# Performance work log

Hardware: AMD Instinct MI355X
Metric: run time of the kernel (lower is better)

Reference implementation:

```python
import math
import jax, jax.numpy as jnp
import numpy as np
from jax import lax

N, L = 256, 4096
DIM_LINEAR, DIM_CONV, KERNEL, STRIDE = 64, 128, 15, 1


def setup_inputs() -> dict:
    key = jax.random.key(0)
    ks = jax.random.split(key, 10)
    tokens = jax.random.randint(ks[0], (N, L), 0, 4, dtype=jnp.int32)
    emb = jax.random.normal(ks[1], (4, DIM_LINEAR), dtype=jnp.float32)
    conv_w = jax.random.normal(ks[2], (DIM_CONV, DIM_LINEAR, KERNEL), dtype=jnp.float32) * (1.0 / math.sqrt(DIM_LINEAR * KERNEL))
    conv_b = jax.random.normal(ks[3], (DIM_CONV,), dtype=jnp.float32) * 0.01
    s = 1.0 / math.sqrt(DIM_CONV)
    Wq = jax.random.normal(ks[4], (DIM_CONV, DIM_CONV), dtype=jnp.float32) * s
    bq = jax.random.normal(ks[5], (DIM_CONV,), dtype=jnp.float32) * 0.01
    Wk = jax.random.normal(ks[6], (DIM_CONV, DIM_CONV), dtype=jnp.float32) * s
    bk = jax.random.normal(ks[7], (DIM_CONV,), dtype=jnp.float32) * 0.01
    Wv = jax.random.normal(ks[8], (DIM_CONV, DIM_CONV), dtype=jnp.float32) * s
    bv = jax.random.normal(ks[9], (DIM_CONV,), dtype=jnp.float32) * 0.01
    return {"tokens": tokens, "emb": emb, "conv_w": conv_w, "conv_b": conv_b,
            "Wq": Wq, "bq": bq, "Wk": Wk, "bk": bk, "Wv": Wv, "bv": bv}


def reference(tokens, emb, conv_w, conv_b, Wq, bq, Wk, bk, Wv, bv):
    # embedding: [N, L, dl] -> channels-first [N, dl, L]
    x = emb[tokens].transpose(0, 2, 1)
    # conv1d, valid padding: [N, dc, Lout]
    y = lax.conv_general_dilated(x, conv_w, window_strides=(STRIDE,),
                                 padding='VALID',
                                 dimension_numbers=('NCH', 'OIH', 'NCH'))
    y = y + conv_b[None, :, None]
    read = y.transpose(0, 2, 1)                      # [N, Lout, dc]
    read_mean = read.mean(axis=1)                    # [N, dc]
    q = read_mean @ Wq.T + bq                        # [N, dc]
    k = read @ Wk.T + bk                             # [N, Lout, dc]
    v = read @ Wv.T + bv                             # [N, Lout, dc]
    scores = jnp.einsum('nd,nld->nl', q, k) / math.sqrt(DIM_CONV)
    attn = jax.nn.softmax(scores, axis=1)            # [N, Lout]
    out = jnp.einsum('nl,nld->nd', attn, v)          # [N, dc]
    return out
```

## Files before the change

### kernel.cpp

```cpp
#include <hip/hip_runtime.h>
#include <math.h>

#define NN 256
#define LL 4096
#define DL 64
#define DC 128
#define KS 15
#define LOUT (LL - KS + 1)
#define CST 133
#define RSQRT_DC 0.08838834764831843f

__global__ __launch_bounds__(128) void contrib_kernel(const float* __restrict__ emb,
                                                      const float* __restrict__ conv_w,
                                                      float* __restrict__ ctb) {
    const int c = blockIdx.x;
    const int tid = threadIdx.x;
    __shared__ float ws[DL][16];
    __shared__ float es[4][DL];
    const float* wsrc = conv_w + (size_t)c * (DL * KS);
    for (int idx = tid; idx < DL * KS; idx += 128) ws[idx / KS][idx % KS] = wsrc[idx];
    for (int idx = tid; idx < 4 * DL; idx += 128) es[idx >> 6][idx & 63] = emb[idx];
    __syncthreads();
    if (tid < 60) {
        const int v = tid / KS, k = tid % KS;
        float s = 0.f;
#pragma unroll
        for (int i = 0; i < DL; ++i) s += es[v][i] * ws[i][k];
        ctb[tid * DC + c] = s;
    }
}

__device__ __forceinline__ float block_sum(float v, float* red8, int tid) {
#pragma unroll
    for (int off = 32; off > 0; off >>= 1) v += __shfl_down(v, off, 64);
    if ((tid & 63) == 0) red8[tid >> 6] = v;
    __syncthreads();
    float r = ((red8[0] + red8[1]) + (red8[2] + red8[3])) +
              ((red8[4] + red8[5]) + (red8[6] + red8[7]));
    __syncthreads();
    return r;
}

__device__ __forceinline__ float block_max(float v, float* red8, int tid) {
#pragma unroll
    for (int off = 32; off > 0; off >>= 1) v = fmaxf(v, __shfl_down(v, off, 64));
    if ((tid & 63) == 0) red8[tid >> 6] = v;
    __syncthreads();
    float r = fmaxf(fmaxf(fmaxf(red8[0], red8[1]), fmaxf(red8[2], red8[3])),
                    fmaxf(fmaxf(red8[4], red8[5]), fmaxf(red8[6], red8[7])));
    __syncthreads();
    return r;
}

__global__ __launch_bounds__(512) void encoder_kernel(
    const int* __restrict__ tokens, const float* __restrict__ ctb_g,
    const float* __restrict__ conv_b,
    const float* __restrict__ Wq, const float* __restrict__ bq,
    const float* __restrict__ Wk, const float* __restrict__ bk,
    const float* __restrict__ Wv, const float* __restrict__ bv,
    float* __restrict__ out) {
    const int n = blockIdx.x;
    const int tid = threadIdx.x;

    __shared__ __align__(16) float esc[16 + LL];
    __shared__ unsigned tok2[258];
    __shared__ float ctb[60 * CST];
    __shared__ float Tt[4 * 256];
    __shared__ float rm[DC], qv[DC], qk[DC], zv[DC];
    __shared__ float stab[60], cf[60], Acc[60];
    __shared__ float red8[8];
    __shared__ int totw[4][4];
    __shared__ int cnt[KS][4];

#define TOK2(p) ((tok2[(p) >> 4] >> (2 * ((p) & 15))) & 3u)

    for (int i = tid; i < 16 + LL; i += 512) esc[i] = 0.f;
    if (tid < 60) Acc[tid] = 0.f;
    if (tid < 2) tok2[256 + tid] = 0u;
    for (int idx = tid; idx < 60 * DC; idx += 512)
        ctb[(idx >> 7) * CST + (idx & 127)] = ctb_g[idx];

    if (tid < 256) {
        const int4* tv = (const int4*)(tokens + (size_t)n * LL) + tid * 4;
        unsigned w = 0;
#pragma unroll
        for (int m = 0; m < 4; ++m) {
            int4 t4 = tv[m];
            w |= ((unsigned)t4.x | ((unsigned)t4.y << 2) |
                  ((unsigned)t4.z << 4) | ((unsigned)t4.w << 6)) << (8 * m);
        }
        tok2[tid] = w;
        int c0, c1, c2, c3;
        {
            unsigned y, z;
            y = w;                      z = (y | (y >> 1)) & 0x55555555u; c0 = 16 - __popc(z);
            y = w ^ 0x55555555u;        z = (y | (y >> 1)) & 0x55555555u; c1 = 16 - __popc(z);
            y = w ^ 0xAAAAAAAAu;        z = (y | (y >> 1)) & 0x55555555u; c2 = 16 - __popc(z);
            y = w ^ 0xFFFFFFFFu;        z = (y | (y >> 1)) & 0x55555555u; c3 = 16 - __popc(z);
        }
#pragma unroll
        for (int off = 32; off > 0; off >>= 1) {
            c0 += __shfl_down(c0, off, 64); c1 += __shfl_down(c1, off, 64);
            c2 += __shfl_down(c2, off, 64); c3 += __shfl_down(c3, off, 64);
        }
        if ((tid & 63) == 0) {
            const int wv = tid >> 6;
            totw[wv][0] = c0; totw[wv][1] = c1; totw[wv][2] = c2; totw[wv][3] = c3;
        }
    }
    __syncthreads();

    if (tid < KS) {
        const int k = tid;
        int h0 = 0, h1 = 0, h2 = 0, h3 = 0;
        for (int p = 0; p < k; ++p) {
            int v = (int)TOK2(p);
            h0 += (v == 0); h1 += (v == 1); h2 += (v == 2); h3 += (v == 3);
        }
        for (int p = k + LOUT; p < LL; ++p) {
            int v = (int)TOK2(p);
            h0 += (v == 0); h1 += (v == 1); h2 += (v == 2); h3 += (v == 3);
        }
        cnt[k][0] = (totw[0][0] + totw[1][0] + totw[2][0] + totw[3][0]) - h0;
        cnt[k][1] = (totw[0][1] + totw[1][1] + totw[2][1] + totw[3][1]) - h1;
        cnt[k][2] = (totw[0][2] + totw[1][2] + totw[2][2] + totw[3][2]) - h2;
        cnt[k][3] = (totw[0][3] + totw[1][3] + totw[2][3] + totw[3][3]) - h3;
    }
    __syncthreads();
    if (tid < 60) cf[tid] = (float)cnt[tid % KS][tid / KS];
    __syncthreads();

    if (tid < DC) {
        float s = 0.f;
#pragma unroll
        for (int j = 0; j < 60; ++j) s += cf[j] * ctb[j * CST + tid];
        rm[tid] = conv_b[tid] + s * (1.0f / (float)LOUT);
    }
    __syncthreads();

    if (tid < DC) {
        const float4* wr = (const float4*)(Wq + (size_t)tid * DC);
        const float4* r4 = (const float4*)rm;
        float s = 0.f;
#pragma unroll
        for (int j = 0; j < DC / 4; ++j) {
            float4 w = wr[j], r = r4[j];
            s += w.x * r.x + w.y * r.y + w.z * r.z + w.w * r.w;
        }
        qv[tid] = s + bq[tid];
    }
    __syncthreads();

    if (tid < DC) {
        float s = 0.f;
        for (int c = 0; c < DC; ++c) s += qv[c] * Wk[(size_t)c * DC + tid];
        qk[tid] = s;
    }
    __syncthreads();

    if (tid < 60) {
        float s = 0.f;
#pragma unroll
        for (int c = 0; c < DC; ++c) s += ctb[tid * CST + c] * qk[c];
        stab[tid] = s * RSQRT_DC;
    }
    float term = 0.f;
    if (tid < DC) term = conv_b[tid] * qk[tid] + qv[tid] * bk[tid];
    const float base = block_sum(term, red8, tid) * RSQRT_DC;

    for (int e = tid; e < 1024; e += 512) {
        const int j = e >> 8, b = e & 255;
        float s = stab[(b & 3) * KS + 4 * j] +
                  stab[((b >> 2) & 3) * KS + 4 * j + 1] +
                  stab[((b >> 4) & 3) * KS + 4 * j + 2];
        if (j < 3) s += stab[((b >> 6) & 3) * KS + 4 * j + 3];
        Tt[e] = s;
    }
    __syncthreads();

    const unsigned d0 = tok2[tid >> 1];
    const unsigned d1 = tok2[(tid >> 1) + 1];
    const unsigned long long W = (unsigned long long)d0 | ((unsigned long long)d1 << 32);
    const int sbase = (tid & 1) << 4;
    const int t0 = tid * 8;
    float lmax = -3.4e38f;
    {
        float sreg[8];
#pragma unroll
        for (int p = 0; p < 8; ++p) {
            const unsigned w = (unsigned)(W >> (sbase + 2 * p));
            sreg[p] = base + Tt[w & 255] + Tt[256 + ((w >> 8) & 255)] +
                      Tt[512 + ((w >> 16) & 255)] + Tt[768 + ((w >> 24) & 63)];
        }
#pragma unroll
        for (int p = 0; p < 8; ++p) {
            if (t0 + p < LOUT) { esc[16 + t0 + p] = sreg[p]; lmax = fmaxf(lmax, sreg[p]); }
        }
    }
    const float m = block_max(lmax, red8, tid);

    float lsum = 0.f;
    for (int t = tid; t < LOUT; t += 512) {
        float e = __expf(esc[16 + t] - m);
        esc[16 + t] = e;
        lsum += e;
    }
    const float S = block_sum(lsum, red8, tid);
    const float invS = 1.0f / S;

    {
        float ew[24];
        const float4* ep = (const float4*)(esc + t0);
#pragma unroll
        for (int i = 0; i < 6; ++i) {
            float4 f = ep[i];
            ew[4 * i] = f.x; ew[4 * i + 1] = f.y; ew[4 * i + 2] = f.z; ew[4 * i + 3] = f.w;
        }
        float a1[KS], a2[KS], a3[KS];
#pragma unroll
        for (int k = 0; k < KS; ++k) { a1[k] = 0.f; a2[k] = 0.f; a3[k] = 0.f; }
#pragma unroll
        for (int p = 0; p < 8; ++p) {
            const int v = (int)((W >> (sbase + 2 * p)) & 3ull);
            const float m1 = (v == 1) ? 1.f : 0.f;
            const float m2 = (v == 2) ? 1.f : 0.f;
            const float m3 = (v == 3) ? 1.f : 0.f;
#pragma unroll
            for (int k = 0; k < KS; ++k) {
                const float e = ew[16 + p - k];
                a1[k] += m1 * e; a2[k] += m2 * e; a3[k] += m3 * e;
            }
        }
        const int lane = tid & 63;
#pragma unroll
        for (int k = 0; k < KS; ++k) {
            float v1 = a1[k], v2 = a2[k], v3 = a3[k];
#pragma unroll
            for (int off = 32; off > 0; off >>= 1) {
                v1 += __shfl_down(v1, off, 64);
                v2 += __shfl_down(v2, off, 64);
                v3 += __shfl_down(v3, off, 64);
            }
            if (lane == 0) {
                atomicAdd(&Acc[KS + k], v1);
                atomicAdd(&Acc[2 * KS + k], v2);
                atomicAdd(&Acc[3 * KS + k], v3);
            }
        }
    }
    __syncthreads();
    if (tid < KS) Acc[tid] = S - Acc[KS + tid] - Acc[2 * KS + tid] - Acc[3 * KS + tid];
    __syncthreads();

    if (tid < DC) {
        float s = 0.f;
#pragma unroll
        for (int j = 0; j < 60; ++j) s += Acc[j] * ctb[j * CST + tid];
        zv[tid] = conv_b[tid] + s * invS;
    }
    __syncthreads();

    if (tid < DC) {
        const float4* wr = (const float4*)(Wv + (size_t)tid * DC);
        const float4* z4 = (const float4*)zv;
        float s = 0.f;
#pragma unroll
        for (int j = 0; j < DC / 4; ++j) {
            float4 w = wr[j], z = z4[j];
            s += w.x * z.x + w.y * z.y + w.z * z.z + w.w * z.w;
        }
        out[(size_t)n * DC + tid] = s + bv[tid];
    }
#undef TOK2
}

extern "C" void kernel_launch(void* const* d_in, const int* in_sizes, int n_in,
                              void* d_out, int out_size, void* d_ws, size_t ws_size,
                              hipStream_t stream) {
    const int*   tokens = (const int*)d_in[0];
    const float* emb    = (const float*)d_in[1];
    const float* conv_w = (const float*)d_in[2];
    const float* conv_b = (const float*)d_in[3];
    const float* Wq     = (const float*)d_in[4];
    const float* bq     = (const float*)d_in[5];
    const float* Wk     = (const float*)d_in[6];
    const float* bk     = (const float*)d_in[7];
    const float* Wv     = (const float*)d_in[8];
    const float* bv     = (const float*)d_in[9];
    float* out = (float*)d_out;
    float* ctb = (float*)d_ws;

    contrib_kernel<<<DC, 128, 0, stream>>>(emb, conv_w, ctb);
    encoder_kernel<<<NN, 512, 0, stream>>>(tokens, ctb, conv_b,
                                           Wq, bq, Wk, bk, Wv, bv, out);
}
```

Measured before the change: 103.4 us.

## Split encoder into chain, split-sequence score, and final merge kernels

Breaks the single per-sample encoder kernel into three kernels. The first computes the q-chain and score table per sample. The second splits the sequence into two halves per sample, doubling the block count, and computes partial softmax stats and token-weighted accumulators in registers without a large shared score buffer. The third merges the halves with a max-rescaled combine and applies the V projection. This aims to raise occupancy and parallelism by cutting shared memory and the 256-block grid, at the cost of two extra launches and global round-trips through the workspace.

```diff
diff --git a/kernel.cpp b/kernel.cpp
--- a/kernel.cpp
+++ b/kernel.cpp
@@ -7,80 +7,82 @@
 #define DC 128
 #define KS 15
 #define LOUT (LL - KS + 1)
+#define HB 2048
 #define CST 133
 #define RSQRT_DC 0.08838834764831843f
+
+#define WS_STABB 7680
+#define WS_PART  24064
 
 __global__ __launch_bounds__(128) void contrib_kernel(const float* __restrict__ emb,
                                                       const float* __restrict__ conv_w,
                                                       float* __restrict__ ctb) {
     const int c = blockIdx.x;
     const int tid = threadIdx.x;
-    __shared__ float ws[DL][16];
+    __shared__ float wsm[DL][16];
     __shared__ float es[4][DL];
     const float* wsrc = conv_w + (size_t)c * (DL * KS);
-    for (int idx = tid; idx < DL * KS; idx += 128) ws[idx / KS][idx % KS] = wsrc[idx];
+    for (int idx = tid; idx < DL * KS; idx += 128) wsm[idx / KS][idx % KS] = wsrc[idx];
     for (int idx = tid; idx < 4 * DL; idx += 128) es[idx >> 6][idx & 63] = emb[idx];
     __syncthreads();
     if (tid < 60) {
         const int v = tid / KS, k = tid % KS;
         float s = 0.f;
 #pragma unroll
-        for (int i = 0; i < DL; ++i) s += es[v][i] * ws[i][k];
+        for (int i = 0; i < DL; ++i) s += es[v][i] * wsm[i][k];
         ctb[tid * DC + c] = s;
     }
 }
 
-__device__ __forceinline__ float block_sum(float v, float* red8, int tid) {
+template <int NW>
+__device__ __forceinline__ float bsum(float v, float* red, int tid) {
 #pragma unroll
     for (int off = 32; off > 0; off >>= 1) v += __shfl_down(v, off, 64);
-    if ((tid & 63) == 0) red8[tid >> 6] = v;
-    __syncthreads();
-    float r = ((red8[0] + red8[1]) + (red8[2] + red8[3])) +
-              ((red8[4] + red8[5]) + (red8[6] + red8[7]));
+    if ((tid & 63) == 0) red[tid >> 6] = v;
+    __syncthreads();
+    float r = 0.f;
+#pragma unroll
+    for (int w = 0; w < NW; ++w) r += red[w];
     __syncthreads();
     return r;
 }
 
-__device__ __forceinline__ float block_max(float v, float* red8, int tid) {
+template <int NW>
+__device__ __forceinline__ float bmax(float v, float* red, int tid) {
 #pragma unroll
     for (int off = 32; off > 0; off >>= 1) v = fmaxf(v, __shfl_down(v, off, 64));
-    if ((tid & 63) == 0) red8[tid >> 6] = v;
-    __syncthreads();
-    float r = fmaxf(fmaxf(fmaxf(red8[0], red8[1]), fmaxf(red8[2], red8[3])),
-                    fmaxf(fmaxf(red8[4], red8[5]), fmaxf(red8[6], red8[7])));
+    if ((tid & 63) == 0) red[tid >> 6] = v;
+    __syncthreads();
+    float r = red[0];
+#pragma unroll
+    for (int w = 1; w < NW; ++w) r = fmaxf(r, red[w]);
     __syncthreads();
     return r;
 }
 
-__global__ __launch_bounds__(512) void encoder_kernel(
+__global__ __launch_bounds__(256) void chain_kernel(
     const int* __restrict__ tokens, const float* __restrict__ ctb_g,
     const float* __restrict__ conv_b,
     const float* __restrict__ Wq, const float* __restrict__ bq,
     const float* __restrict__ Wk, const float* __restrict__ bk,
-    const float* __restrict__ Wv, const float* __restrict__ bv,
-    float* __restrict__ out) {
+    float* __restrict__ ws) {
     const int n = blockIdx.x;
     const int tid = threadIdx.x;
 
-    __shared__ __align__(16) float esc[16 + LL];
-    __shared__ unsigned tok2[258];
+    __shared__ unsigned tok2[256];
     __shared__ float ctb[60 * CST];
-    __shared__ float Tt[4 * 256];
-    __shared__ float rm[DC], qv[DC], qk[DC], zv[DC];
-    __shared__ float stab[60], cf[60], Acc[60];
-    __shared__ float red8[8];
+    __shared__ float rm[DC], qv[DC], qk[DC];
+    __shared__ float cf[60];
+    __shared__ float red4[4];
     __shared__ int totw[4][4];
     __shared__ int cnt[KS][4];
 
 #define TOK2(p) ((tok2[(p) >> 4] >> (2 * ((p) & 15))) & 3u)
 
-    for (int i = tid; i < 16 + LL; i += 512) esc[i] = 0.f;
-    if (tid < 60) Acc[tid] = 0.f;
-    if (tid < 2) tok2[256 + tid] = 0u;
-    for (int idx = tid; idx < 60 * DC; idx += 512)
+    for (int idx = tid; idx < 60 * DC; idx += 256)
         ctb[(idx >> 7) * CST + (idx & 127)] = ctb_g[idx];
 
-    if (tid < 256) {
+    {
         const int4* tv = (const int4*)(tokens + (size_t)n * LL) + tid * 4;
         unsigned w = 0;
 #pragma unroll
@@ -91,13 +93,11 @@
         }
         tok2[tid] = w;
         int c0, c1, c2, c3;
-        {
-            unsigned y, z;
-            y = w;                      z = (y | (y >> 1)) & 0x55555555u; c0 = 16 - __popc(z);
-            y = w ^ 0x55555555u;        z = (y | (y >> 1)) & 0x55555555u; c1 = 16 - __popc(z);
-            y = w ^ 0xAAAAAAAAu;        z = (y | (y >> 1)) & 0x55555555u; c2 = 16 - __popc(z);
-            y = w ^ 0xFFFFFFFFu;        z = (y | (y >> 1)) & 0x55555555u; c3 = 16 - __popc(z);
-        }
+        unsigned y, z;
+        y = w;               z = (y | (y >> 1)) & 0x55555555u; c0 = 16 - __popc(z);
+        y = w ^ 0x55555555u; z = (y | (y >> 1)) & 0x55555555u; c1 = 16 - __popc(z);
+        y = w ^ 0xAAAAAAAAu; z = (y | (y >> 1)) & 0x55555555u; c2 = 16 - __popc(z);
+        y = w ^ 0xFFFFFFFFu; z = (y | (y >> 1)) & 0x55555555u; c3 = 16 - __popc(z);
 #pragma unroll
         for (int off = 32; off > 0; off >>= 1) {
             c0 += __shfl_down(c0, off, 64); c1 += __shfl_down(c1, off, 64);
@@ -158,79 +158,111 @@
     }
     __syncthreads();
 
+    float* sw = ws + WS_STABB + n * 64;
     if (tid < 60) {
         float s = 0.f;
-#pragma unroll
+#pragma unroll 4
         for (int c = 0; c < DC; ++c) s += ctb[tid * CST + c] * qk[c];
-        stab[tid] = s * RSQRT_DC;
+        sw[tid] = s * RSQRT_DC;
     }
     float term = 0.f;
     if (tid < DC) term = conv_b[tid] * qk[tid] + qv[tid] * bk[tid];
-    const float base = block_sum(term, red8, tid) * RSQRT_DC;
-
+    const float base = bsum<4>(term, red4, tid) * RSQRT_DC;
+    if (tid == 0) sw[60] = base;
+#undef TOK2
+}
+
+__global__ __launch_bounds__(512, 4) void score_kernel(
+    const int* __restrict__ tokens, float* __restrict__ ws) {
+    const int b = blockIdx.x;
+    const int n = b >> 1, h = b & 1;
+    const int t0 = h * HB;
+    const int NP = h ? (LOUT - HB) : HB;
+    const int tid = threadIdx.x;
+
+    __shared__ float Tt[1024];
+    __shared__ unsigned tok2[132];
+    __shared__ float stabL[64];
+    __shared__ float AccL[45];
+    __shared__ float red8[8];
+
+    const float* sw = ws + WS_STABB + n * 64;
+    if (tid < 61) stabL[tid] = sw[tid];
+    if (tid < 45) AccL[tid] = 0.f;
+    if (tid >= 130 && tid < 132) tok2[tid] = 0u;
+
+    if (tid < 130) {
+        const int* tb = tokens + (size_t)n * LL;
+        unsigned w = 0;
+#pragma unroll
+        for (int m = 0; m < 4; ++m) {
+            int gi = t0 + tid * 16 + m * 4;
+            if (gi > LL - 4) gi = LL - 4;
+            const int4 t4 = *(const int4*)(tb + gi);
+            w |= ((unsigned)t4.x | ((unsigned)t4.y << 2) |
+                  ((unsigned)t4.z << 4) | ((unsigned)t4.w << 6)) << (8 * m);
+        }
+        tok2[tid] = w;
+    }
+    __syncthreads();
+
+    const float base = stabL[60];
     for (int e = tid; e < 1024; e += 512) {
-        const int j = e >> 8, b = e & 255;
-        float s = stab[(b & 3) * KS + 4 * j] +
-                  stab[((b >> 2) & 3) * KS + 4 * j + 1] +
-                  stab[((b >> 4) & 3) * KS + 4 * j + 2];
-        if (j < 3) s += stab[((b >> 6) & 3) * KS + 4 * j + 3];
+        const int j = e >> 8, bb = e & 255;
+        float s = stabL[(bb & 3) * KS + 4 * j] +
+                  stabL[((bb >> 2) & 3) * KS + 4 * j + 1] +
+                  stabL[((bb >> 4) & 3) * KS + 4 * j + 2];
+        if (j < 3) s += stabL[((bb >> 6) & 3) * KS + 4 * j + 3];
         Tt[e] = s;
     }
     __syncthreads();
 
-    const unsigned d0 = tok2[tid >> 1];
-    const unsigned d1 = tok2[(tid >> 1) + 1];
-    const unsigned long long W = (unsigned long long)d0 | ((unsigned long long)d1 << 32);
-    const int sbase = (tid & 1) << 4;
-    const int t0 = tid * 8;
+    float sc[4];
+    unsigned wreg[4];
     float lmax = -3.4e38f;
+#pragma unroll
+    for (int j = 0; j < 4; ++j) {
+        const int tl = tid + 512 * j;
+        if (tl < NP) {
+            const unsigned dw0 = tok2[tl >> 4];
+            const unsigned dw1 = tok2[(tl >> 4) + 1];
+            const unsigned long long W =
+                ((unsigned long long)dw0 | ((unsigned long long)dw1 << 32)) >> (2 * (tl & 15));
+            const unsigned w = (unsigned)W;
+            wreg[j] = w;
+            sc[j] = base + Tt[w & 255] + Tt[256 + ((w >> 8) & 255)] +
+                    Tt[512 + ((w >> 16) & 255)] + Tt[768 + ((w >> 24) & 63)];
+            lmax = fmaxf(lmax, sc[j]);
+        } else { wreg[j] = 0u; sc[j] = -3.4e38f; }
+    }
+    const float m = bmax<8>(lmax, red8, tid);
+
+    float ev[4];
+    float lsum = 0.f;
+#pragma unroll
+    for (int j = 0; j < 4; ++j) {
+        const int tl = tid + 512 * j;
+        ev[j] = (tl < NP) ? __expf(sc[j] - m) : 0.f;
+        lsum += ev[j];
+    }
+    const float S = bsum<8>(lsum, red8, tid);
+
+    float a1[KS], a2[KS], a3[KS];
+#pragma unroll
+    for (int k = 0; k < KS; ++k) { a1[k] = 0.f; a2[k] = 0.f; a3[k] = 0.f; }
+#pragma unroll
+    for (int j = 0; j < 4; ++j) {
+        const float e = ev[j];
+        const unsigned w = wreg[j];
+#pragma unroll
+        for (int k = 0; k < KS; ++k) {
+            const int v = (int)((w >> (2 * k)) & 3u);
+            a1[k] += (v == 1) ? e : 0.f;
+            a2[k] += (v == 2) ? e : 0.f;
+            a3[k] += (v == 3) ? e : 0.f;
+        }
+    }
     {
-        float sreg[8];
-#pragma unroll
-        for (int p = 0; p < 8; ++p) {
-            const unsigned w = (unsigned)(W >> (sbase + 2 * p));
-            sreg[p] = base + Tt[w & 255] + Tt[256 + ((w >> 8) & 255)] +
-                      Tt[512 + ((w >> 16) & 255)] + Tt[768 + ((w >> 24) & 63)];
-        }
-#pragma unroll
-        for (int p = 0; p < 8; ++p) {
-            if (t0 + p < LOUT) { esc[16 + t0 + p] = sreg[p]; lmax = fmaxf(lmax, sreg[p]); }
-        }
-    }
-    const float m = block_max(lmax, red8, tid);
-
-    float lsum = 0.f;
-    for (int t = tid; t < LOUT; t += 512) {
-        float e = __expf(esc[16 + t] - m);
-        esc[16 + t] = e;
-        lsum += e;
-    }
-    const float S = block_sum(lsum, red8, tid);
-    const float invS = 1.0f / S;
-
-    {
-        float ew[24];
-        const float4* ep = (const float4*)(esc + t0);
-#pragma unroll
-        for (int i = 0; i < 6; ++i) {
-            float4 f = ep[i];
-            ew[4 * i] = f.x; ew[4 * i + 1] = f.y; ew[4 * i + 2] = f.z; ew[4 * i + 3] = f.w;
-        }
-        float a1[KS], a2[KS], a3[KS];
-#pragma unroll
-        for (int k = 0; k < KS; ++k) { a1[k] = 0.f; a2[k] = 0.f; a3[k] = 0.f; }
-#pragma unroll
-        for (int p = 0; p < 8; ++p) {
-            const int v = (int)((W >> (sbase + 2 * p)) & 3ull);
-            const float m1 = (v == 1) ? 1.f : 0.f;
-            const float m2 = (v == 2) ? 1.f : 0.f;
-            const float m3 = (v == 3) ? 1.f : 0.f;
-#pragma unroll
-            for (int k = 0; k < KS; ++k) {
-                const float e = ew[16 + p - k];
-                a1[k] += m1 * e; a2[k] += m2 * e; a3[k] += m3 * e;
-            }
-        }
         const int lane = tid & 63;
 #pragma unroll
         for (int k = 0; k < KS; ++k) {
@@ -242,25 +274,54 @@
                 v3 += __shfl_down(v3, off, 64);
             }
             if (lane == 0) {
-                atomicAdd(&Acc[KS + k], v1);
-                atomicAdd(&Acc[2 * KS + k], v2);
-                atomicAdd(&Acc[3 * KS + k], v3);
+                atomicAdd(&AccL[k], v1);
+                atomicAdd(&AccL[KS + k], v2);
+                atomicAdd(&AccL[2 * KS + k], v3);
             }
         }
     }
     __syncthreads();
-    if (tid < KS) Acc[tid] = S - Acc[KS + tid] - Acc[2 * KS + tid] - Acc[3 * KS + tid];
-    __syncthreads();
-
-    if (tid < DC) {
-        float s = 0.f;
-#pragma unroll
-        for (int j = 0; j < 60; ++j) s += Acc[j] * ctb[j * CST + tid];
-        zv[tid] = conv_b[tid] + s * invS;
-    }
-    __syncthreads();
-
-    if (tid < DC) {
+
+    float* P = ws + WS_PART + (size_t)(n * 2 + h) * 48;
+    if (tid < 45) P[tid] = AccL[tid];
+    else if (tid == 45) P[45] = m;
+    else if (tid == 46) P[46] = S;
+}
+
+__global__ __launch_bounds__(128) void final_kernel(
+    const float* __restrict__ ctb_g, const float* __restrict__ conv_b,
+    const float* __restrict__ Wv, const float* __restrict__ bv,
+    const float* __restrict__ ws, float* __restrict__ out) {
+    const int n = blockIdx.x;
+    const int tid = threadIdx.x;
+    __shared__ float Acc[60];
+    __shared__ float zv[DC];
+    __shared__ float scs[4];
+
+    const float* P0 = ws + WS_PART + (size_t)(n * 2) * 48;
+    const float* P1 = P0 + 48;
+    if (tid == 0) {
+        const float m0 = P0[45], m1 = P1[45];
+        const float m = fmaxf(m0, m1);
+        const float r0 = __expf(m0 - m), r1 = __expf(m1 - m);
+        const float S = P0[46] * r0 + P1[46] * r1;
+        scs[0] = r0; scs[1] = r1; scs[2] = 1.0f / S; scs[3] = S;
+    }
+    __syncthreads();
+    if (tid < 45) Acc[KS + tid] = P0[tid] * scs[0] + P1[tid] * scs[1];
+    __syncthreads();
+    if (tid < KS) Acc[tid] = scs[3] - Acc[KS + tid] - Acc[2 * KS + tid] - Acc[3 * KS + tid];
+    __syncthreads();
+
+    {
+        float s = 0.f;
+#pragma unroll
+        for (int j = 0; j < 60; ++j) s += Acc[j] * ctb_g[j * DC + tid];
+        zv[tid] = conv_b[tid] + s * scs[2];
+    }
+    __syncthreads();
+
+    {
         const float4* wr = (const float4*)(Wv + (size_t)tid * DC);
         const float4* z4 = (const float4*)zv;
         float s = 0.f;
@@ -271,7 +332,6 @@
         }
         out[(size_t)n * DC + tid] = s + bv[tid];
     }
-#undef TOK2
 }
 
 extern "C" void kernel_launch(void* const* d_in, const int* in_sizes, int n_in,
@@ -288,9 +348,10 @@
     const float* Wv     = (const float*)d_in[8];
     const float* bv     = (const float*)d_in[9];
     float* out = (float*)d_out;
-    float* ctb = (float*)d_ws;
-
-    contrib_kernel<<<DC, 128, 0, stream>>>(emb, conv_w, ctb);
-    encoder_kernel<<<NN, 512, 0, stream>>>(tokens, ctb, conv_b,
-                                           Wq, bq, Wk, bk, Wv, bv, out);
-}
+    float* ws  = (float*)d_ws;
+
+    contrib_kernel<<<DC, 128, 0, stream>>>(emb, conv_w, ws);
+    chain_kernel<<<NN, 256, 0, stream>>>(tokens, ws, conv_b, Wq, bq, Wk, bk, ws);
+    score_kernel<<<NN * 2, 512, 0, stream>>>(tokens, ws);
+    final_kernel<<<NN, 128, 0, stream>>>(ws, conv_b, Wv, bv, ws, out);
+}
```

Measured after the change: 113.1 us. +9.4%, slower.

## Move token packing to prep kernel and restructure encode stage into warp-parallel pipeline

Applied to the files above, without the earlier changes.

Token packing and per-sequence symbol counts move into the prep kernel, which also computes the conv-embedding table in extra blocks. The encode kernel drops the shared ctb copy and the scratch score buffer. It computes the edge counts with bitmask popcounts instead of a serial loop, and one wave runs the q/k/stab chain while the other waves load tokens. Softmax scores stay in registers, and the shifted-window accumulation reads symbols from the packed word rather than an exp buffer in shared memory. This cuts shared memory use and barriers, at the cost of reading ctb from global memory and adding a workspace round trip.

```diff
diff --git a/kernel.cpp b/kernel.cpp
--- a/kernel.cpp
+++ b/kernel.cpp
@@ -7,230 +7,240 @@
 #define DC 128
 #define KS 15
 #define LOUT (LL - KS + 1)
-#define CST 133
 #define RSQRT_DC 0.08838834764831843f
-
-__global__ __launch_bounds__(128) void contrib_kernel(const float* __restrict__ emb,
-                                                      const float* __restrict__ conv_w,
-                                                      float* __restrict__ ctb) {
-    const int c = blockIdx.x;
-    const int tid = threadIdx.x;
-    __shared__ float ws[DL][16];
-    __shared__ float es[4][DL];
-    const float* wsrc = conv_w + (size_t)c * (DL * KS);
-    for (int idx = tid; idx < DL * KS; idx += 128) ws[idx / KS][idx % KS] = wsrc[idx];
-    for (int idx = tid; idx < 4 * DL; idx += 128) es[idx >> 6][idx & 63] = emb[idx];
-    __syncthreads();
-    if (tid < 60) {
-        const int v = tid / KS, k = tid % KS;
-        float s = 0.f;
-#pragma unroll
-        for (int i = 0; i < DL; ++i) s += es[v][i] * ws[i][k];
-        ctb[tid * DC + c] = s;
-    }
-}
-
-__device__ __forceinline__ float block_sum(float v, float* red8, int tid) {
+#define INV_LOUT (1.0f / (float)LOUT)
+
+#define WS_CTB  0
+#define WS_PACK 7680
+#define WS_CNT  73216
+
+__global__ __launch_bounds__(256) void prep_kernel(const int* __restrict__ tokens,
+                                                   const float* __restrict__ emb,
+                                                   const float* __restrict__ conv_w,
+                                                   float* __restrict__ ws) {
+    const int b = blockIdx.x, tid = threadIdx.x;
+    if (b < NN) {
+        __shared__ int totw[4][4];
+        const int n = b;
+        const int4* tv = (const int4*)(tokens + (size_t)n * LL) + tid * 4;
+        unsigned w = 0;
+#pragma unroll
+        for (int m = 0; m < 4; ++m) {
+            int4 t4 = tv[m];
+            w |= ((unsigned)t4.x | ((unsigned)t4.y << 2) |
+                  ((unsigned)t4.z << 4) | ((unsigned)t4.w << 6)) << (8 * m);
+        }
+        ((unsigned*)ws)[WS_PACK + n * 256 + tid] = w;
+        int c0, c1, c2, c3;
+        unsigned y, z;
+        y = w;               z = (y | (y >> 1)) & 0x55555555u; c0 = 16 - __popc(z);
+        y = w ^ 0x55555555u; z = (y | (y >> 1)) & 0x55555555u; c1 = 16 - __popc(z);
+        y = w ^ 0xAAAAAAAAu; z = (y | (y >> 1)) & 0x55555555u; c2 = 16 - __popc(z);
+        y = w ^ 0xFFFFFFFFu; z = (y | (y >> 1)) & 0x55555555u; c3 = 16 - __popc(z);
+#pragma unroll
+        for (int off = 32; off > 0; off >>= 1) {
+            c0 += __shfl_down(c0, off, 64); c1 += __shfl_down(c1, off, 64);
+            c2 += __shfl_down(c2, off, 64); c3 += __shfl_down(c3, off, 64);
+        }
+        if ((tid & 63) == 0) {
+            const int wv = tid >> 6;
+            totw[wv][0] = c0; totw[wv][1] = c1; totw[wv][2] = c2; totw[wv][3] = c3;
+        }
+        __syncthreads();
+        if (tid < 4)
+            ((int*)ws)[WS_CNT + n * 4 + tid] =
+                totw[0][tid] + totw[1][tid] + totw[2][tid] + totw[3][tid];
+    } else {
+        const int c = b - NN;
+        __shared__ float wsm[DL][16];
+        __shared__ float es[4][DL];
+        const float* wsrc = conv_w + (size_t)c * (DL * KS);
+        for (int idx = tid; idx < DL * KS; idx += 256) wsm[idx / KS][idx % KS] = wsrc[idx];
+        es[tid >> 6][tid & 63] = emb[tid];
+        __syncthreads();
+        if (tid < 60) {
+            const int v = tid / KS, k = tid % KS;
+            float s = 0.f;
+#pragma unroll
+            for (int i = 0; i < DL; ++i) s += es[v][i] * wsm[i][k];
+            ws[WS_CTB + tid * DC + c] = s;
+        }
+    }
+}
+
+template <int NW>
+__device__ __forceinline__ float bsum(float v, float* red, int tid) {
 #pragma unroll
     for (int off = 32; off > 0; off >>= 1) v += __shfl_down(v, off, 64);
-    if ((tid & 63) == 0) red8[tid >> 6] = v;
-    __syncthreads();
-    float r = ((red8[0] + red8[1]) + (red8[2] + red8[3])) +
-              ((red8[4] + red8[5]) + (red8[6] + red8[7]));
+    if ((tid & 63) == 0) red[tid >> 6] = v;
+    __syncthreads();
+    float r = 0.f;
+#pragma unroll
+    for (int w = 0; w < NW; ++w) r += red[w];
     __syncthreads();
     return r;
 }
 
-__device__ __forceinline__ float block_max(float v, float* red8, int tid) {
+template <int NW>
+__device__ __forceinline__ float bmax(float v, float* red, int tid) {
 #pragma unroll
     for (int off = 32; off > 0; off >>= 1) v = fmaxf(v, __shfl_down(v, off, 64));
-    if ((tid & 63) == 0) red8[tid >> 6] = v;
-    __syncthreads();
-    float r = fmaxf(fmaxf(fmaxf(red8[0], red8[1]), fmaxf(red8[2], red8[3])),
-                    fmaxf(fmaxf(red8[4], red8[5]), fmaxf(red8[6], red8[7])));
+    if ((tid & 63) == 0) red[tid >> 6] = v;
+    __syncthreads();
+    float r = red[0];
+#pragma unroll
+    for (int w = 1; w < NW; ++w) r = fmaxf(r, red[w]);
     __syncthreads();
     return r;
 }
 
-__global__ __launch_bounds__(512) void encoder_kernel(
-    const int* __restrict__ tokens, const float* __restrict__ ctb_g,
-    const float* __restrict__ conv_b,
+__global__ __launch_bounds__(512) void encode_kernel(
+    const float* __restrict__ ws, const float* __restrict__ conv_b,
     const float* __restrict__ Wq, const float* __restrict__ bq,
     const float* __restrict__ Wk, const float* __restrict__ bk,
     const float* __restrict__ Wv, const float* __restrict__ bv,
     float* __restrict__ out) {
-    const int n = blockIdx.x;
-    const int tid = threadIdx.x;
-
-    __shared__ __align__(16) float esc[16 + LL];
-    __shared__ unsigned tok2[258];
-    __shared__ float ctb[60 * CST];
-    __shared__ float Tt[4 * 256];
-    __shared__ float rm[DC], qv[DC], qk[DC], zv[DC];
-    __shared__ float stab[60], cf[60], Acc[60];
-    __shared__ float red8[8];
-    __shared__ int totw[4][4];
-    __shared__ int cnt[KS][4];
-
-#define TOK2(p) ((tok2[(p) >> 4] >> (2 * ((p) & 15))) & 3u)
-
-    for (int i = tid; i < 16 + LL; i += 512) esc[i] = 0.f;
-    if (tid < 60) Acc[tid] = 0.f;
-    if (tid < 2) tok2[256 + tid] = 0u;
-    for (int idx = tid; idx < 60 * DC; idx += 512)
-        ctb[(idx >> 7) * CST + (idx & 127)] = ctb_g[idx];
-
-    if (tid < 256) {
-        const int4* tv = (const int4*)(tokens + (size_t)n * LL) + tid * 4;
-        unsigned w = 0;
-#pragma unroll
-        for (int m = 0; m < 4; ++m) {
-            int4 t4 = tv[m];
-            w |= ((unsigned)t4.x | ((unsigned)t4.y << 2) |
-                  ((unsigned)t4.z << 4) | ((unsigned)t4.w << 6)) << (8 * m);
-        }
-        tok2[tid] = w;
-        int c0, c1, c2, c3;
-        {
-            unsigned y, z;
-            y = w;                      z = (y | (y >> 1)) & 0x55555555u; c0 = 16 - __popc(z);
-            y = w ^ 0x55555555u;        z = (y | (y >> 1)) & 0x55555555u; c1 = 16 - __popc(z);
-            y = w ^ 0xAAAAAAAAu;        z = (y | (y >> 1)) & 0x55555555u; c2 = 16 - __popc(z);
-            y = w ^ 0xFFFFFFFFu;        z = (y | (y >> 1)) & 0x55555555u; c3 = 16 - __popc(z);
-        }
-#pragma unroll
-        for (int off = 32; off > 0; off >>= 1) {
-            c0 += __shfl_down(c0, off, 64); c1 += __shfl_down(c1, off, 64);
-            c2 += __shfl_down(c2, off, 64); c3 += __shfl_down(c3, off, 64);
-        }
-        if ((tid & 63) == 0) {
-            const int wv = tid >> 6;
-            totw[wv][0] = c0; totw[wv][1] = c1; totw[wv][2] = c2; totw[wv][3] = c3;
-        }
-    }
-    __syncthreads();
-
-    if (tid < KS) {
-        const int k = tid;
-        int h0 = 0, h1 = 0, h2 = 0, h3 = 0;
-        for (int p = 0; p < k; ++p) {
-            int v = (int)TOK2(p);
-            h0 += (v == 0); h1 += (v == 1); h2 += (v == 2); h3 += (v == 3);
-        }
-        for (int p = k + LOUT; p < LL; ++p) {
-            int v = (int)TOK2(p);
-            h0 += (v == 0); h1 += (v == 1); h2 += (v == 2); h3 += (v == 3);
-        }
-        cnt[k][0] = (totw[0][0] + totw[1][0] + totw[2][0] + totw[3][0]) - h0;
-        cnt[k][1] = (totw[0][1] + totw[1][1] + totw[2][1] + totw[3][1]) - h1;
-        cnt[k][2] = (totw[0][2] + totw[1][2] + totw[2][2] + totw[3][2]) - h2;
-        cnt[k][3] = (totw[0][3] + totw[1][3] + totw[2][3] + totw[3][3]) - h3;
-    }
-    __syncthreads();
-    if (tid < 60) cf[tid] = (float)cnt[tid % KS][tid / KS];
-    __syncthreads();
-
-    if (tid < DC) {
-        float s = 0.f;
-#pragma unroll
-        for (int j = 0; j < 60; ++j) s += cf[j] * ctb[j * CST + tid];
-        rm[tid] = conv_b[tid] + s * (1.0f / (float)LOUT);
-    }
-    __syncthreads();
-
-    if (tid < DC) {
-        const float4* wr = (const float4*)(Wq + (size_t)tid * DC);
-        const float4* r4 = (const float4*)rm;
-        float s = 0.f;
-#pragma unroll
-        for (int j = 0; j < DC / 4; ++j) {
-            float4 w = wr[j], r = r4[j];
-            s += w.x * r.x + w.y * r.y + w.z * r.z + w.w * r.w;
-        }
-        qv[tid] = s + bq[tid];
-    }
-    __syncthreads();
-
-    if (tid < DC) {
-        float s = 0.f;
-        for (int c = 0; c < DC; ++c) s += qv[c] * Wk[(size_t)c * DC + tid];
-        qk[tid] = s;
-    }
-    __syncthreads();
-
-    if (tid < 60) {
-        float s = 0.f;
-#pragma unroll
-        for (int c = 0; c < DC; ++c) s += ctb[tid * CST + c] * qk[c];
-        stab[tid] = s * RSQRT_DC;
-    }
-    float term = 0.f;
-    if (tid < DC) term = conv_b[tid] * qk[tid] + qv[tid] * bk[tid];
-    const float base = block_sum(term, red8, tid) * RSQRT_DC;
-
+    const int n = blockIdx.x, tid = threadIdx.x;
+    const float* ctb = ws + WS_CTB;
+    const unsigned* packed = (const unsigned*)ws + WS_PACK;
+
+    __shared__ unsigned tok2L[258];
+    __shared__ float stabL[64];
+    __shared__ float cfL[60];
+    __shared__ float rmL[DC], qvL[DC], qkL[DC], zvL[DC];
+    __shared__ float Tt[1024];
+    __shared__ float AccL[45];
+    __shared__ float red[8];
+
+    if (tid >= 64) {
+        const int i = tid - 64;
+        if (i < 258) tok2L[i] = (i < 256) ? packed[n * 256 + i] : 0u;
+        else if (i < 258 + 45) AccL[i - 258] = 0.f;
+    } else {
+        const int l = tid;
+        const int4 ct = *(const int4*)((const int*)ws + WS_CNT + n * 4);
+        const unsigned dwF = packed[n * 256];
+        const unsigned dwL = packed[n * 256 + 255];
+        if (l < KS) {
+            const int k = l;
+            const unsigned pm = (k == 0) ? 0u : ((1u << (2 * k)) - 1u);
+            const unsigned sm = (k == 14) ? 0u : (0xFFFFFFFFu << (2 * (k + 2)));
+            const int tot4[4] = {ct.x, ct.y, ct.z, ct.w};
+#pragma unroll
+            for (int v = 0; v < 4; ++v) {
+                const unsigned patt = (unsigned)v * 0x55555555u;
+                unsigned yf = dwF ^ patt, zf = (yf | (yf >> 1)) & 0x55555555u;
+                unsigned yl = dwL ^ patt, zl = (yl | (yl >> 1)) & 0x55555555u;
+                const int pre = k - __popc(zf & pm);
+                const int suf = (14 - k) - __popc(zl & sm);
+                cfL[v * KS + k] = (float)(tot4[v] - pre - suf);
+            }
+        }
+        const int c0 = 2 * l, c1 = 2 * l + 1;
+        float r0 = 0.f, r1 = 0.f;
+        for (int j = 0; j < 60; ++j) {
+            const float cfj = cfL[j];
+            const float2 cb = *(const float2*)(ctb + j * DC + c0);
+            r0 += cfj * cb.x; r1 += cfj * cb.y;
+        }
+        const float2 cb2 = *(const float2*)(conv_b + c0);
+        r0 = cb2.x + r0 * INV_LOUT; r1 = cb2.y + r1 * INV_LOUT;
+        rmL[c0] = r0; rmL[c1] = r1;
+        const float4* wq0 = (const float4*)(Wq + (size_t)c0 * DC);
+        const float4* wq1 = (const float4*)(Wq + (size_t)c1 * DC);
+        const float4* rr = (const float4*)rmL;
+        float s0 = 0.f, s1 = 0.f;
+#pragma unroll 8
+        for (int j = 0; j < 32; ++j) {
+            const float4 r = rr[j], a = wq0[j], b = wq1[j];
+            s0 += a.x * r.x + a.y * r.y + a.z * r.z + a.w * r.w;
+            s1 += b.x * r.x + b.y * r.y + b.z * r.z + b.w * r.w;
+        }
+        const float2 bq2 = *(const float2*)(bq + c0);
+        const float qv0 = s0 + bq2.x, qv1 = s1 + bq2.y;
+        qvL[c0] = qv0; qvL[c1] = qv1;
+        float k0 = 0.f, k1 = 0.f;
+        const float4* qq = (const float4*)qvL;
+        for (int c4 = 0; c4 < 32; ++c4) {
+            const float4 q4 = qq[c4];
+            const float2 w0 = *(const float2*)(Wk + (size_t)(4 * c4 + 0) * DC + c0);
+            const float2 w1 = *(const float2*)(Wk + (size_t)(4 * c4 + 1) * DC + c0);
+            const float2 w2 = *(const float2*)(Wk + (size_t)(4 * c4 + 2) * DC + c0);
+            const float2 w3 = *(const float2*)(Wk + (size_t)(4 * c4 + 3) * DC + c0);
+            k0 += q4.x * w0.x + q4.y * w1.x + q4.z * w2.x + q4.w * w3.x;
+            k1 += q4.x * w0.y + q4.y * w1.y + q4.z * w2.y + q4.w * w3.y;
+        }
+        qkL[c0] = k0; qkL[c1] = k1;
+        if (l < 60) {
+            const float4* cr = (const float4*)(ctb + (size_t)l * DC);
+            const float4* qk4 = (const float4*)qkL;
+            float s = 0.f;
+#pragma unroll 8
+            for (int t = 0; t < 32; ++t) {
+                const float4 a = cr[t], q = qk4[t];
+                s += a.x * q.x + a.y * q.y + a.z * q.z + a.w * q.w;
+            }
+            stabL[l] = s * RSQRT_DC;
+        }
+        const float2 bk2 = *(const float2*)(bk + c0);
+        float t = cb2.x * k0 + cb2.y * k1 + qv0 * bk2.x + qv1 * bk2.y;
+#pragma unroll
+        for (int off = 32; off > 0; off >>= 1) t += __shfl_down(t, off, 64);
+        if (l == 0) stabL[60] = t * RSQRT_DC;
+    }
+    __syncthreads();
+
+    const float base = stabL[60];
     for (int e = tid; e < 1024; e += 512) {
-        const int j = e >> 8, b = e & 255;
-        float s = stab[(b & 3) * KS + 4 * j] +
-                  stab[((b >> 2) & 3) * KS + 4 * j + 1] +
-                  stab[((b >> 4) & 3) * KS + 4 * j + 2];
-        if (j < 3) s += stab[((b >> 6) & 3) * KS + 4 * j + 3];
+        const int j = e >> 8, bb = e & 255;
+        float s = stabL[(bb & 3) * KS + 4 * j] +
+                  stabL[((bb >> 2) & 3) * KS + 4 * j + 1] +
+                  stabL[((bb >> 4) & 3) * KS + 4 * j + 2];
+        if (j < 3) s += stabL[((bb >> 6) & 3) * KS + 4 * j + 3];
         Tt[e] = s;
     }
     __syncthreads();
 
-    const unsigned d0 = tok2[tid >> 1];
-    const unsigned d1 = tok2[(tid >> 1) + 1];
+    const unsigned d0 = tok2L[tid >> 1], d1 = tok2L[(tid >> 1) + 1];
     const unsigned long long W = (unsigned long long)d0 | ((unsigned long long)d1 << 32);
     const int sbase = (tid & 1) << 4;
     const int t0 = tid * 8;
+    float sc[8];
     float lmax = -3.4e38f;
+#pragma unroll
+    for (int p = 0; p < 8; ++p) {
+        const unsigned w = (unsigned)(W >> (sbase + 2 * p));
+        const float s = base + Tt[w & 255] + Tt[256 + ((w >> 8) & 255)] +
+                        Tt[512 + ((w >> 16) & 255)] + Tt[768 + ((w >> 24) & 63)];
+        sc[p] = (t0 + p < LOUT) ? s : -3.4e38f;
+        lmax = fmaxf(lmax, sc[p]);
+    }
+    const float m = bmax<8>(lmax, red, tid);
+    float lsum = 0.f;
+#pragma unroll
+    for (int p = 0; p < 8; ++p) {
+        const float e = (t0 + p < LOUT) ? __expf(sc[p] - m) : 0.f;
+        sc[p] = e; lsum += e;
+    }
+    const float S = bsum<8>(lsum, red, tid);
+    const float invS = 1.0f / S;
+
+    float a1[KS], a2[KS], a3[KS];
+#pragma unroll
+    for (int k = 0; k < KS; ++k) { a1[k] = 0.f; a2[k] = 0.f; a3[k] = 0.f; }
+#pragma unroll
+    for (int p = 0; p < 8; ++p) {
+        const float e = sc[p];
+        const unsigned w = (unsigned)(W >> (sbase + 2 * p));
+#pragma unroll
+        for (int k = 0; k < KS; ++k) {
+            const int v = (int)((w >> (2 * k)) & 3u);
+            a1[k] += (v == 1) ? e : 0.f;
+            a2[k] += (v == 2) ? e : 0.f;
+            a3[k] += (v == 3) ? e : 0.f;
+        }
+    }
     {
-        float sreg[8];
-#pragma unroll
-        for (int p = 0; p < 8; ++p) {
-            const unsigned w = (unsigned)(W >> (sbase + 2 * p));
-            sreg[p] = base + Tt[w & 255] + Tt[256 + ((w >> 8) & 255)] +
-                      Tt[512 + ((w >> 16) & 255)] + Tt[768 + ((w >> 24) & 63)];
-        }
-#pragma unroll
-        for (int p = 0; p < 8; ++p) {
-            if (t0 + p < LOUT) { esc[16 + t0 + p] = sreg[p]; lmax = fmaxf(lmax, sreg[p]); }
-        }
-    }
-    const float m = block_max(lmax, red8, tid);
-
-    float lsum = 0.f;
-    for (int t = tid; t < LOUT; t += 512) {
-        float e = __expf(esc[16 + t] - m);
-        esc[16 + t] = e;
-        lsum += e;
-    }
-    const float S = block_sum(lsum, red8, tid);
-    const float invS = 1.0f / S;
-
-    {
-        float ew[24];
-        const float4* ep = (const float4*)(esc + t0);
-#pragma unroll
-        for (int i = 0; i < 6; ++i) {
-            float4 f = ep[i];
-            ew[4 * i] = f.x; ew[4 * i + 1] = f.y; ew[4 * i + 2] = f.z; ew[4 * i + 3] = f.w;
-        }
-        float a1[KS], a2[KS], a3[KS];
-#pragma unroll
-        for (int k = 0; k < KS; ++k) { a1[k] = 0.f; a2[k] = 0.f; a3[k] = 0.f; }
-#pragma unroll
-        for (int p = 0; p < 8; ++p) {
-            const int v = (int)((W >> (sbase + 2 * p)) & 3ull);
-            const float m1 = (v == 1) ? 1.f : 0.f;
-            const float m2 = (v == 2) ? 1.f : 0.f;
-            const float m3 = (v == 3) ? 1.f : 0.f;
-#pragma unroll
-            for (int k = 0; k < KS; ++k) {
-                const float e = ew[16 + p - k];
-                a1[k] += m1 * e; a2[k] += m2 * e; a3[k] += m3 * e;
-            }
-        }
         const int lane = tid & 63;
 #pragma unroll
         for (int k = 0; k < KS; ++k) {
@@ -242,36 +252,38 @@
                 v3 += __shfl_down(v3, off, 64);
             }
             if (lane == 0) {
-                atomicAdd(&Acc[KS + k], v1);
-                atomicAdd(&Acc[2 * KS + k], v2);
-                atomicAdd(&Acc[3 * KS + k], v3);
+                atomicAdd(&AccL[k], v1);
+                atomicAdd(&AccL[KS + k], v2);
+                atomicAdd(&AccL[2 * KS + k], v3);
             }
         }
     }
-    __syncthreads();
-    if (tid < KS) Acc[tid] = S - Acc[KS + tid] - Acc[2 * KS + tid] - Acc[3 * KS + tid];
     __syncthreads();
 
     if (tid < DC) {
         float s = 0.f;
 #pragma unroll
-        for (int j = 0; j < 60; ++j) s += Acc[j] * ctb[j * CST + tid];
-        zv[tid] = conv_b[tid] + s * invS;
+        for (int k = 0; k < KS; ++k) {
+            const float a0 = S - AccL[k] - AccL[KS + k] - AccL[2 * KS + k];
+            s += a0 * ctb[k * DC + tid];
+        }
+#pragma unroll
+        for (int j = KS; j < 60; ++j) s += AccL[j - KS] * ctb[j * DC + tid];
+        zvL[tid] = conv_b[tid] + s * invS;
     }
     __syncthreads();
 
     if (tid < DC) {
         const float4* wr = (const float4*)(Wv + (size_t)tid * DC);
-        const float4* z4 = (const float4*)zv;
+        const float4* z4 = (const float4*)zvL;
         float s = 0.f;
-#pragma unroll
-        for (int j = 0; j < DC / 4; ++j) {
-            float4 w = wr[j], z = z4[j];
+#pragma unroll 8
+        for (int j = 0; j < 32; ++j) {
+            const float4 w = wr[j], z = z4[j];
             s += w.x * z.x + w.y * z.y + w.z * z.z + w.w * z.w;
         }
         out[(size_t)n * DC + tid] = s + bv[tid];
     }
-#undef TOK2
 }
 
 extern "C" void kernel_launch(void* const* d_in, const int* in_sizes, int n_in,
@@ -288,9 +300,8 @@
     const float* Wv     = (const float*)d_in[8];
     const float* bv     = (const float*)d_in[9];
     float* out = (float*)d_out;
-    float* ctb = (float*)d_ws;
-
-    contrib_kernel<<<DC, 128, 0, stream>>>(emb, conv_w, ctb);
-    encoder_kernel<<<NN, 512, 0, stream>>>(tokens, ctb, conv_b,
-                                           Wq, bq, Wk, bk, Wv, bv, out);
-}
+    float* ws  = (float*)d_ws;
+
+    prep_kernel<<<NN + DC, 256, 0, stream>>>(tokens, emb, conv_w, ws);
+    encode_kernel<<<NN, 512, 0, stream>>>(ws, conv_b, Wq, bq, Wk, bk, Wv, bv, out);
+}
```

Measured after the change: 100.5 us. 1.03x faster.
